# Performance work log

Measured on AMD Instinct MI355X. Metric: run time of the kernel, lower is better.

Reference implementation:

```python
import jax, jax.numpy as jnp
import numpy as np

SQRT_2_OVER_PI = 0.7978845608028654

def _gelu_tanh(m):
    inner = SQRT_2_OVER_PI * (m + 0.044715 * m * m * m)
    return 0.5 * m * (1.0 + jnp.tanh(inner))

def setup_inputs() -> dict:
    key = jax.random.key(0)
    k1, k2, k3, k4 = jax.random.split(key, 4)
    M, N, O = 16384, 4096, 16384
    x = jax.random.normal(k1, (M, N), dtype=jnp.float32)
    weight = jax.random.normal(k2, (O, N), dtype=jnp.float32)
    bias = jax.random.normal(k3, (O,), dtype=jnp.float32)
    subtract = jax.random.normal(k4, (O,), dtype=jnp.float32)
    return {"x": x, "weight": weight, "bias": bias, "subtract": subtract, "out_features": O}

def reference(x, weight, bias, subtract, out_features):
    # Parameter-only precompute (recompute_cache): c_i = sum_j W[j,i],
    # col_sum_bias = sum_j (bias_j - subtract_j)
    c = weight.sum(axis=0)                     # [N]
    col_sum_bias = (bias - subtract).sum()     # scalar
    # Per-row collapsed Linear -> subtract -> mean (logsumexp over 1 elem = identity)
    row_sum = x @ c + col_sum_bias             # [M]
    m = row_sum / out_features                 # [M]
    g = _gelu_tanh(m)                          # [M]
    return x + g[:, None]                      # residual broadcast over features
```

## Files before the change

kernel.cpp:

```cpp
#include <hip/hip_runtime.h>
#include <math.h>

#define THREADS 256
#define CHUNKS 512

typedef int v4i __attribute__((ext_vector_type(4)));

__device__ __forceinline__ float4 ntload4(const float* p) {
    v4i t = __builtin_nontemporal_load(reinterpret_cast<const v4i*>(p));
    float4 r;
    r.x = __int_as_float(t.x); r.y = __int_as_float(t.y);
    r.z = __int_as_float(t.z); r.w = __int_as_float(t.w);
    return r;
}
__device__ __forceinline__ void ntstore4(float* p, const float4 v) {
    v4i t;
    t.x = __float_as_int(v.x); t.y = __float_as_int(v.y);
    t.z = __float_as_int(v.z); t.w = __float_as_int(v.w);
    __builtin_nontemporal_store(t, reinterpret_cast<v4i*>(p));
}

__device__ __forceinline__ float gelu_fast(float m) {
    const float inner = 0.7978845608028654f * (m + 0.044715f * m * m * m);
    return m / (1.0f + __expf(-2.0f * inner));
}

__global__ __launch_bounds__(THREADS)
void colsum_partials_kernel(const float* __restrict__ W, float* __restrict__ partials,
                            int O, int N, int rows_per_chunk) {
    int col = (blockIdx.x * THREADS + threadIdx.x) * 4;
    if (col >= N) return;
    int r0 = blockIdx.y * rows_per_chunk;
    int r1 = r0 + rows_per_chunk; if (r1 > O) r1 = O;
    float ax = 0.f, ay = 0.f, az = 0.f, aw = 0.f;
    #pragma unroll 4
    for (int r = r0; r < r1; ++r) {
        const float4 v = ntload4(W + (size_t)r * N + col);
        ax += v.x; ay += v.y; az += v.z; aw += v.w;
    }
    ntstore4(partials + (size_t)blockIdx.y * N + col, make_float4(ax, ay, az, aw));
}

template<int CH>
__global__ __launch_bounds__(THREADS)
void reduce_bias_kernel(const float* __restrict__ partials,
                        const float* __restrict__ bias, const float* __restrict__ sub,
                        float* __restrict__ c, float* __restrict__ cb,
                        int N, int O) {
    if ((int)blockIdx.x == (int)gridDim.x - 1) {
        float s = 0.f;
        for (int i = threadIdx.x; i < O; i += THREADS) s += bias[i] - sub[i];
        #pragma unroll
        for (int off = 32; off > 0; off >>= 1) s += __shfl_down(s, off, 64);
        __shared__ float lds[THREADS / 64];
        if ((threadIdx.x & 63) == 0) lds[threadIdx.x >> 6] = s;
        __syncthreads();
        if (threadIdx.x == 0) {
            float t = 0.f;
            #pragma unroll
            for (int w = 0; w < THREADS / 64; ++w) t += lds[w];
            *cb = t;
        }
        return;
    }
    const int col = (blockIdx.x * THREADS + threadIdx.x) * 4;
    if (col >= N) return;
    float ax = 0.f, ay = 0.f, az = 0.f, aw = 0.f;
    #pragma unroll 8
    for (int k = 0; k < CH; ++k) {
        const float4 v = *reinterpret_cast<const float4*>(partials + (size_t)k * N + col);
        ax += v.x; ay += v.y; az += v.z; aw += v.w;
    }
    *reinterpret_cast<float4*>(c + col) = make_float4(ax, ay, az, aw);
}

__global__ __launch_bounds__(THREADS)
void reduce_bias_rt_kernel(const float* __restrict__ partials,
                           const float* __restrict__ bias, const float* __restrict__ sub,
                           float* __restrict__ c, float* __restrict__ cb,
                           int N, int O, int chunks) {
    if ((int)blockIdx.x == (int)gridDim.x - 1) {
        float s = 0.f;
        for (int i = threadIdx.x; i < O; i += THREADS) s += bias[i] - sub[i];
        #pragma unroll
        for (int off = 32; off > 0; off >>= 1) s += __shfl_down(s, off, 64);
        __shared__ float lds[THREADS / 64];
        if ((threadIdx.x & 63) == 0) lds[threadIdx.x >> 6] = s;
        __syncthreads();
        if (threadIdx.x == 0) {
            float t = 0.f;
            #pragma unroll
            for (int w = 0; w < THREADS / 64; ++w) t += lds[w];
            *cb = t;
        }
        return;
    }
    const int col = (blockIdx.x * THREADS + threadIdx.x) * 4;
    if (col >= N) return;
    float ax = 0.f, ay = 0.f, az = 0.f, aw = 0.f;
    for (int k = 0; k < chunks; ++k) {
        const float4 v = *reinterpret_cast<const float4*>(partials + (size_t)k * N + col);
        ax += v.x; ay += v.y; az += v.z; aw += v.w;
    }
    *reinterpret_cast<float4*>(c + col) = make_float4(ax, ay, az, aw);
}

template<int VPL>
__global__ __launch_bounds__(THREADS)
void row_wave_kernel(const float* __restrict__ x, const float* __restrict__ c,
                     const float* __restrict__ cb, const int* __restrict__ of_ptr,
                     float* __restrict__ out, int M, int N) {
    const int wave = threadIdx.x >> 6;
    const int lane = threadIdx.x & 63;
    const int row = blockIdx.x * (THREADS / 64) + wave;
    if (row >= M) return;
    const size_t base = (size_t)row * N;

    float4 xv[VPL];
    float partial = 0.f;
    #pragma unroll
    for (int k = 0; k < VPL; ++k) {
        const int idx = (k * 64 + lane) * 4;
        const float4 xx = ntload4(x + base + idx);
        const float4 cc = *reinterpret_cast<const float4*>(c + idx);
        xv[k] = xx;
        partial += xx.x * cc.x + xx.y * cc.y + xx.z * cc.z + xx.w * cc.w;
    }

    #pragma unroll
    for (int off = 1; off < 64; off <<= 1) partial += __shfl_xor(partial, off, 64);

    const float g = gelu_fast((partial + *cb) / (float)(*of_ptr));

    #pragma unroll
    for (int k = 0; k < VPL; ++k) {
        const int idx = (k * 64 + lane) * 4;
        const float4 xx = xv[k];
        ntstore4(out + base + idx, make_float4(xx.x + g, xx.y + g, xx.z + g, xx.w + g));
    }
}

__global__ __launch_bounds__(THREADS)
void row_fused_generic_kernel(const float* __restrict__ x, const float* __restrict__ c,
                              const float* __restrict__ cb, const int* __restrict__ of_ptr,
                              float* __restrict__ out, int N) {
    const size_t base = (size_t)blockIdx.x * N;
    float partial = 0.f;
    for (int i = threadIdx.x; i < N; i += THREADS) partial += x[base + i] * c[i];
    #pragma unroll
    for (int off = 32; off > 0; off >>= 1) partial += __shfl_down(partial, off, 64);
    __shared__ float lds[THREADS / 64];
    if ((threadIdx.x & 63) == 0) lds[threadIdx.x >> 6] = partial;
    __syncthreads();
    float rs = *cb;
    #pragma unroll
    for (int w = 0; w < THREADS / 64; ++w) rs += lds[w];
    const float g = gelu_fast(rs / (float)(*of_ptr));
    for (int i = threadIdx.x; i < N; i += THREADS) out[base + i] = x[base + i] + g;
}

extern "C" void kernel_launch(void* const* d_in, const int* in_sizes, int n_in,
                              void* d_out, int out_size, void* d_ws, size_t ws_size,
                              hipStream_t stream) {
    const float* x    = (const float*)d_in[0];
    const float* W    = (const float*)d_in[1];
    const float* bias = (const float*)d_in[2];
    const float* sub  = (const float*)d_in[3];
    const int* of_ptr = (const int*)d_in[4];

    const int O = in_sizes[2];
    const int N = (int)((long long)in_sizes[1] / O);
    const int M = (int)((long long)in_sizes[0] / N);

    float* ws = (float*)d_ws;
    float* c  = ws;
    float* cb = ws + N;
    float* partials = ws + N + 64;

    const int colblocks = (N + THREADS * 4 - 1) / (THREADS * 4);

    int chunks = CHUNKS;
    {
        long long maxChunks = ((long long)(ws_size / sizeof(float)) - N - 64) / N;
        while (chunks > maxChunks && chunks > 8) chunks >>= 1;
    }
    const int rows_per_chunk = (O + chunks - 1) / chunks;

    dim3 g1(colblocks, chunks);
    colsum_partials_kernel<<<g1, THREADS, 0, stream>>>(W, partials, O, N, rows_per_chunk);

    if (chunks == 512) {
        reduce_bias_kernel<512><<<colblocks + 1, THREADS, 0, stream>>>(
            partials, bias, sub, c, cb, N, O);
    } else if (chunks == 256) {
        reduce_bias_kernel<256><<<colblocks + 1, THREADS, 0, stream>>>(
            partials, bias, sub, c, cb, N, O);
    } else if (chunks == 128) {
        reduce_bias_kernel<128><<<colblocks + 1, THREADS, 0, stream>>>(
            partials, bias, sub, c, cb, N, O);
    } else {
        reduce_bias_rt_kernel<<<colblocks + 1, THREADS, 0, stream>>>(
            partials, bias, sub, c, cb, N, O, chunks);
    }

    const int waves_per_block = THREADS / 64;
    const int G = (M + waves_per_block - 1) / waves_per_block;
    if (N == 4096) {
        row_wave_kernel<16><<<G, THREADS, 0, stream>>>(x, c, cb, of_ptr, (float*)d_out, M, N);
    } else if (N == 2048) {
        row_wave_kernel<8><<<G, THREADS, 0, stream>>>(x, c, cb, of_ptr, (float*)d_out, M, N);
    } else if (N == 8192) {
        row_wave_kernel<32><<<G, THREADS, 0, stream>>>(x, c, cb, of_ptr, (float*)d_out, M, N);
    } else {
        row_fused_generic_kernel<<<M, THREADS, 0, stream>>>(x, c, cb, of_ptr, (float*)d_out, N);
    }
}
```

Before: 173.1 us.

## Fuse colsum, reduction and row pass into one cooperative persistent kernel

Replaces the three-kernel sequence (column-sum partials, reduce plus bias sum, row GELU residual) with a single cooperative kernel that uses grid-wide syncs between phases. The grid is sized from occupancy, and the row phase runs as a persistent grid-stride loop over rows. This is meant to remove launch overhead and inter-kernel idle gaps. In exchange it adds grid barrier cost, limits the number of blocks for latency hiding, and falls back to the old path if the cooperative launch fails.

```diff
diff --git a/kernel.cpp b/kernel.cpp
--- a/kernel.cpp
+++ b/kernel.cpp
@@ -1,8 +1,13 @@
 #include <hip/hip_runtime.h>
+#include <hip/hip_cooperative_groups.h>
 #include <math.h>
 
+namespace cg = cooperative_groups;
+
 #define THREADS 256
-#define CHUNKS 512
+#define NT 4096
+#define COLB 4
+#define VPL 16
 
 typedef int v4i __attribute__((ext_vector_type(4)));
 
@@ -23,6 +28,83 @@
 __device__ __forceinline__ float gelu_fast(float m) {
     const float inner = 0.7978845608028654f * (m + 0.044715f * m * m * m);
     return m / (1.0f + __expf(-2.0f * inner));
+}
+
+__global__ __launch_bounds__(THREADS, 4)
+void fused_all(const float* __restrict__ x, const float* __restrict__ W,
+               const float* __restrict__ bias, const float* __restrict__ sub,
+               const int* __restrict__ of_ptr, float* __restrict__ out,
+               float* __restrict__ partials, float* __restrict__ c,
+               float* __restrict__ cb, int M, int O, int chunks, int rows_per_chunk) {
+    const int t = threadIdx.x;
+    const int b = blockIdx.x;
+    cg::grid_group grid = cg::this_grid();
+
+    {
+        const int cx = b & (COLB - 1);
+        const int cy = b >> 2;
+        if (cy < chunks) {
+            const int col = (cx * THREADS + t) * 4;
+            int r0 = cy * rows_per_chunk;
+            int r1 = r0 + rows_per_chunk; if (r1 > O) r1 = O;
+            float ax = 0.f, ay = 0.f, az = 0.f, aw = 0.f;
+            for (int r = r0; r < r1; ++r) {
+                const float4 v = ntload4(W + (size_t)r * NT + col);
+                ax += v.x; ay += v.y; az += v.z; aw += v.w;
+            }
+            *reinterpret_cast<float4*>(partials + (size_t)cy * NT + col) =
+                make_float4(ax, ay, az, aw);
+        }
+    }
+    grid.sync();
+
+    if (b < NT / THREADS) {
+        const int col = b * THREADS + t;
+        float a = 0.f;
+        for (int k = 0; k < chunks; ++k) a += partials[(size_t)k * NT + col];
+        c[col] = a;
+    } else if (b == NT / THREADS) {
+        float s = 0.f;
+        for (int i = t; i < O; i += THREADS) s += bias[i] - sub[i];
+        #pragma unroll
+        for (int off = 32; off > 0; off >>= 1) s += __shfl_down(s, off, 64);
+        __shared__ float lds[THREADS / 64];
+        if ((t & 63) == 0) lds[t >> 6] = s;
+        __syncthreads();
+        if (t == 0) cb[0] = lds[0] + lds[1] + lds[2] + lds[3];
+    }
+    grid.sync();
+
+    const float cbv    = cb[0];
+    const float inv_of = 1.0f / (float)(of_ptr[0]);
+    const int wave = t >> 6;
+    const int lane = t & 63;
+    const int nwaves = gridDim.x * (THREADS / 64);
+
+    for (int row = b * (THREADS / 64) + wave; row < M; row += nwaves) {
+        const size_t base = (size_t)row * NT;
+        float4 xv[VPL];
+        float partial = 0.f;
+        #pragma unroll
+        for (int k = 0; k < VPL; ++k) {
+            const int idx = (k * 64 + lane) * 4;
+            const float4 xx = ntload4(x + base + idx);
+            const float4 cc = *reinterpret_cast<const float4*>(c + idx);
+            xv[k] = xx;
+            partial += xx.x * cc.x + xx.y * cc.y + xx.z * cc.z + xx.w * cc.w;
+        }
+        #pragma unroll
+        for (int off = 1; off < 64; off <<= 1) partial += __shfl_xor(partial, off, 64);
+
+        const float g = gelu_fast((partial + cbv) * inv_of);
+
+        #pragma unroll
+        for (int k = 0; k < VPL; ++k) {
+            const int idx = (k * 64 + lane) * 4;
+            const float4 xx = xv[k];
+            ntstore4(out + base + idx, make_float4(xx.x + g, xx.y + g, xx.z + g, xx.w + g));
+        }
+    }
 }
 
 __global__ __launch_bounds__(THREADS)
@@ -38,15 +120,15 @@
         const float4 v = ntload4(W + (size_t)r * N + col);
         ax += v.x; ay += v.y; az += v.z; aw += v.w;
     }
-    ntstore4(partials + (size_t)blockIdx.y * N + col, make_float4(ax, ay, az, aw));
-}
-
-template<int CH>
-__global__ __launch_bounds__(THREADS)
-void reduce_bias_kernel(const float* __restrict__ partials,
-                        const float* __restrict__ bias, const float* __restrict__ sub,
-                        float* __restrict__ c, float* __restrict__ cb,
-                        int N, int O) {
+    *reinterpret_cast<float4*>(partials + (size_t)blockIdx.y * N + col) =
+        make_float4(ax, ay, az, aw);
+}
+
+__global__ __launch_bounds__(THREADS)
+void reduce_bias_rt_kernel(const float* __restrict__ partials,
+                           const float* __restrict__ bias, const float* __restrict__ sub,
+                           float* __restrict__ c, float* __restrict__ cb,
+                           int N, int O, int chunks) {
     if ((int)blockIdx.x == (int)gridDim.x - 1) {
         float s = 0.f;
         for (int i = threadIdx.x; i < O; i += THREADS) s += bias[i] - sub[i];
@@ -66,38 +148,6 @@
     const int col = (blockIdx.x * THREADS + threadIdx.x) * 4;
     if (col >= N) return;
     float ax = 0.f, ay = 0.f, az = 0.f, aw = 0.f;
-    #pragma unroll 8
-    for (int k = 0; k < CH; ++k) {
-        const float4 v = *reinterpret_cast<const float4*>(partials + (size_t)k * N + col);
-        ax += v.x; ay += v.y; az += v.z; aw += v.w;
-    }
-    *reinterpret_cast<float4*>(c + col) = make_float4(ax, ay, az, aw);
-}
-
-__global__ __launch_bounds__(THREADS)
-void reduce_bias_rt_kernel(const float* __restrict__ partials,
-                           const float* __restrict__ bias, const float* __restrict__ sub,
-                           float* __restrict__ c, float* __restrict__ cb,
-                           int N, int O, int chunks) {
-    if ((int)blockIdx.x == (int)gridDim.x - 1) {
-        float s = 0.f;
-        for (int i = threadIdx.x; i < O; i += THREADS) s += bias[i] - sub[i];
-        #pragma unroll
-        for (int off = 32; off > 0; off >>= 1) s += __shfl_down(s, off, 64);
-        __shared__ float lds[THREADS / 64];
-        if ((threadIdx.x & 63) == 0) lds[threadIdx.x >> 6] = s;
-        __syncthreads();
-        if (threadIdx.x == 0) {
-            float t = 0.f;
-            #pragma unroll
-            for (int w = 0; w < THREADS / 64; ++w) t += lds[w];
-            *cb = t;
-        }
-        return;
-    }
-    const int col = (blockIdx.x * THREADS + threadIdx.x) * 4;
-    if (col >= N) return;
-    float ax = 0.f, ay = 0.f, az = 0.f, aw = 0.f;
     for (int k = 0; k < chunks; ++k) {
         const float4 v = *reinterpret_cast<const float4*>(partials + (size_t)k * N + col);
         ax += v.x; ay += v.y; az += v.z; aw += v.w;
@@ -105,7 +155,7 @@
     *reinterpret_cast<float4*>(c + col) = make_float4(ax, ay, az, aw);
 }
 
-template<int VPL>
+template<int KVPL>
 __global__ __launch_bounds__(THREADS)
 void row_wave_kernel(const float* __restrict__ x, const float* __restrict__ c,
                      const float* __restrict__ cb, const int* __restrict__ of_ptr,
@@ -115,25 +165,21 @@
     const int row = blockIdx.x * (THREADS / 64) + wave;
     if (row >= M) return;
     const size_t base = (size_t)row * N;
-
-    float4 xv[VPL];
+    float4 xv[KVPL];
     float partial = 0.f;
     #pragma unroll
-    for (int k = 0; k < VPL; ++k) {
+    for (int k = 0; k < KVPL; ++k) {
         const int idx = (k * 64 + lane) * 4;
         const float4 xx = ntload4(x + base + idx);
         const float4 cc = *reinterpret_cast<const float4*>(c + idx);
         xv[k] = xx;
         partial += xx.x * cc.x + xx.y * cc.y + xx.z * cc.z + xx.w * cc.w;
     }
-
     #pragma unroll
     for (int off = 1; off < 64; off <<= 1) partial += __shfl_xor(partial, off, 64);
-
     const float g = gelu_fast((partial + *cb) / (float)(*of_ptr));
-
-    #pragma unroll
-    for (int k = 0; k < VPL; ++k) {
+    #pragma unroll
+    for (int k = 0; k < KVPL; ++k) {
         const int idx = (k * 64 + lane) * 4;
         const float4 xx = xv[k];
         ntstore4(out + base + idx, make_float4(xx.x + g, xx.y + g, xx.z + g, xx.w + g));
@@ -177,31 +223,45 @@
     float* cb = ws + N;
     float* partials = ws + N + 64;
 
+    const long long maxChunks = ((long long)(ws_size / sizeof(float)) - N - 64) / N;
+
+    if (N == NT) {
+        int blocksPerCU = 0, numCU = 0, dev = 0;
+        hipError_t qe = hipOccupancyMaxActiveBlocksPerMultiprocessor(
+            &blocksPerCU, fused_all, THREADS, 0);
+        hipGetDevice(&dev);
+        hipDeviceGetAttribute(&numCU, hipDeviceAttributeMultiprocessorCount, dev);
+        if (qe == hipSuccess && blocksPerCU >= 1 && numCU >= 1) {
+            long long G = (long long)blocksPerCU * numCU;
+            if (G > 1024) G = 1024;
+            G &= ~(long long)(COLB - 1);
+            long long chunksLL = G / COLB;
+            if (chunksLL > maxChunks) chunksLL = maxChunks;
+            int chunks = (int)chunksLL;
+            if (G >= COLB * (NT / THREADS) + COLB && chunks >= 8) {
+                int rpc = (O + chunks - 1) / chunks;
+                float* outp = (float*)d_out;
+                int Gi = (int)G;
+                void* args[] = { (void*)&x, (void*)&W, (void*)&bias, (void*)&sub,
+                                 (void*)&of_ptr, (void*)&outp, (void*)&partials,
+                                 (void*)&c, (void*)&cb, (void*)&M, (void*)&O,
+                                 (void*)&chunks, (void*)&rpc };
+                hipError_t e = hipLaunchCooperativeKernel(
+                    (void*)fused_all, dim3(Gi), dim3(THREADS), args, 0, stream);
+                if (e == hipSuccess) return;
+            }
+        }
+    }
+
     const int colblocks = (N + THREADS * 4 - 1) / (THREADS * 4);
-
-    int chunks = CHUNKS;
-    {
-        long long maxChunks = ((long long)(ws_size / sizeof(float)) - N - 64) / N;
-        while (chunks > maxChunks && chunks > 8) chunks >>= 1;
-    }
+    int chunks = 512;
+    while (chunks > maxChunks && chunks > 8) chunks >>= 1;
     const int rows_per_chunk = (O + chunks - 1) / chunks;
 
     dim3 g1(colblocks, chunks);
     colsum_partials_kernel<<<g1, THREADS, 0, stream>>>(W, partials, O, N, rows_per_chunk);
-
-    if (chunks == 512) {
-        reduce_bias_kernel<512><<<colblocks + 1, THREADS, 0, stream>>>(
-            partials, bias, sub, c, cb, N, O);
-    } else if (chunks == 256) {
-        reduce_bias_kernel<256><<<colblocks + 1, THREADS, 0, stream>>>(
-            partials, bias, sub, c, cb, N, O);
-    } else if (chunks == 128) {
-        reduce_bias_kernel<128><<<colblocks + 1, THREADS, 0, stream>>>(
-            partials, bias, sub, c, cb, N, O);
-    } else {
-        reduce_bias_rt_kernel<<<colblocks + 1, THREADS, 0, stream>>>(
-            partials, bias, sub, c, cb, N, O, chunks);
-    }
+    reduce_bias_rt_kernel<<<colblocks + 1, THREADS, 0, stream>>>(
+        partials, bias, sub, c, cb, N, O, chunks);
 
     const int waves_per_block = THREADS / 64;
     const int G = (M + waves_per_block - 1) / waves_per_block;
```

Measured after the change: 318.7 us. +84.1%, slower.
